# Optimization experiments

Measured on AMD Instinct MI355X. Metric: run time of the kernel, lower is better.

## Reference

```python
import jax, jax.numpy as jnp
import numpy as np

B, T, C = 8, 2048, 1024

def setup_inputs() -> dict:
    key = jax.random.key(0)
    ks = jax.random.split(key, 5)
    s_in = 1.0 / np.sqrt(C)
    s3 = 1.0 / np.sqrt(3 * C)
    return {
        'x': jax.random.normal(ks[0], (B, T, C), dtype=jnp.float32),
        'w_attn': jax.random.normal(ks[1], (C, 3 * C), dtype=jnp.float32) * s_in,
        'b_attn': jnp.zeros((3 * C,), dtype=jnp.float32),
        'w_proj': jax.random.normal(ks[2], (C, C), dtype=jnp.float32) * s_in,
        'b_proj': jnp.zeros((C,), dtype=jnp.float32),
    }

def reference(x, w_attn, b_attn, w_proj, b_proj):
    Bv, Tv, Cv = x.shape
    qkv = x @ w_attn + b_attn                      # [B,T,3C]
    q, k, v = jnp.split(qkv, 3, axis=-1)           # each [B,T,C]
    # causal additive mask, matching original -1e10 constant
    mask = jnp.where(jnp.tril(jnp.ones((Tv, Tv), dtype=jnp.bool_)), 0.0, -10000000000.0)
    attn = jnp.einsum('btc,bsc->bts', q, k) / jnp.sqrt(jnp.float32(Cv)) + mask
    attn = jax.nn.softmax(attn, axis=-1)           # [B,T,T]
    out = jnp.einsum('bts,bsc->btc', attn, v)      # [B,T,C]
    return out @ w_proj + b_proj
```

## Files before the change

### kernel.cpp

```cpp
#include <hip/hip_runtime.h>
#include <hip/hip_bf16.h>

typedef __hip_bfloat16 bf16_t;
typedef __attribute__((ext_vector_type(8))) __bf16 bf16x8;
typedef __attribute__((ext_vector_type(4))) float f32x4;
typedef __attribute__((ext_vector_type(8))) unsigned short u16x8;


__device__ __forceinline__ void gld_lds16(const void* g, void* l) {
    __builtin_amdgcn_global_load_lds(
        (const __attribute__((address_space(1))) unsigned int*)g,
        (__attribute__((address_space(3))) unsigned int*)l,
        16, 0, 0);
}

__device__ __forceinline__ unsigned short bf16_bits(float x) {
    bf16_t b = __float2bfloat16(x);
    return *reinterpret_cast<unsigned short*>(&b);
}


__global__ __launch_bounds__(256) void cvt_f32_bf16_kernel(
    const float* __restrict__ in, bf16_t* __restrict__ out, long n4) {
    long stride = (long)gridDim.x * blockDim.x;
    for (long i = (long)blockIdx.x * blockDim.x + threadIdx.x; i < n4; i += stride) {
        float4 v = reinterpret_cast<const float4*>(in)[i];
        ushort4 o;
        o.x = bf16_bits(v.x);
        o.y = bf16_bits(v.y);
        o.z = bf16_bits(v.z);
        o.w = bf16_bits(v.w);
        reinterpret_cast<ushort4*>(out)[i] = o;
    }
}


__global__ __launch_bounds__(256) void transpose_f32_bf16_kernel(
    const float* __restrict__ in, bf16_t* __restrict__ out, long ldin, long ldout) {
    __shared__ float tile[32][33];
    int c0 = blockIdx.x * 32, r0 = blockIdx.y * 32;
    int x = threadIdx.x;
#pragma unroll
    for (int yy = 0; yy < 4; ++yy) {
        int y = threadIdx.y + yy * 8;
        tile[y][x] = in[(long)(r0 + y) * ldin + c0 + x];
    }
    __syncthreads();
#pragma unroll
    for (int yy = 0; yy < 4; ++yy) {
        int y = threadIdx.y + yy * 8;
        out[(long)(c0 + y) * ldout + r0 + x] = __float2bfloat16(tile[x][y]);
    }
}

__global__ __launch_bounds__(256) void transpose_bf16_kernel(
    const bf16_t* __restrict__ in, bf16_t* __restrict__ out,
    long ldin, long ldout, long sIn, long sOut) {
    __shared__ bf16_t tile[32][33];
    in  += (long)blockIdx.z * sIn;
    out += (long)blockIdx.z * sOut;
    int c0 = blockIdx.x * 32, r0 = blockIdx.y * 32;
    int x = threadIdx.x;
#pragma unroll
    for (int yy = 0; yy < 4; ++yy) {
        int y = threadIdx.y + yy * 8;
        tile[y][x] = in[(long)(r0 + y) * ldin + c0 + x];
    }
    __syncthreads();
#pragma unroll
    for (int yy = 0; yy < 4; ++yy) {
        int y = threadIdx.y + yy * 8;
        out[(long)(c0 + y) * ldout + r0 + x] = tile[x][y];
    }
}


__global__ __launch_bounds__(512, 2) void gemm256_kernel(
    const bf16_t* __restrict__ A, const bf16_t* __restrict__ Bt,
    void* __restrict__ Cp, const float* __restrict__ bias,
    float scale, int K,
    long lda, long ldb, long ldc,
    long strideA, long strideB, long strideC,
    int mtiles, int causal_skip, int causal_klimit, int c_f32)
{
    __shared__ __align__(16) bf16_t As[2][256 * 32];
    __shared__ __align__(16) bf16_t Bs[2][256 * 32];

    int nwg = gridDim.x;
    int bid = blockIdx.x;
    int swz = (bid & 7) * (nwg >> 3) + (bid >> 3);
    int bm_t = swz % mtiles, bn_t = swz / mtiles;
    if (causal_skip && bn_t > bm_t) return;
    long bm0 = (long)bm_t * 256, bn0 = (long)bn_t * 256;

    int b = blockIdx.z;
    const char* Ab = (const char*)(A + (long)b * strideA + bm0 * lda);
    const char* Bb = (const char*)(Bt + (long)b * strideB + bn0 * ldb);
    long ldab = lda * 2, ldbb = ldb * 2;

    int tid = threadIdx.x, wave = tid >> 6, lane = tid & 63;
    int wm = wave >> 2, wn = wave & 3;
    int lr = lane & 15, kc = lane >> 4;

    int Kend = K;
    if (causal_klimit) { long kl = bm0 + 256; Kend = (kl < (long)K) ? (int)kl : K; }
    int NT = Kend >> 5;
    int NI = NT >> 1;

    int offw = wave * 1024 + lane * 16;
    int rih  = offw >> 6;
    long colswz = (long)(((lane & 3) ^ ((rih >> 1) & 3)) << 4);
    long rowbA0 = (long)rih * ldab, rowbA1 = (long)(rih + 128) * ldab;
    long rowbB0 = (long)rih * ldbb, rowbB1 = (long)(rih + 128) * ldbb;
    int ldsoff = wave * 1024;

    auto STA = [&](int t, int h, int buf) {
        gld_lds16(Ab + (h ? rowbA1 : rowbA0) + (long)t * 64 + colswz,
                  (char*)&As[buf][0] + h * 8192 + ldsoff);
    };
    auto STB = [&](int t, int h, int buf) {
        gld_lds16(Bb + (h ? rowbB1 : rowbB0) + (long)t * 64 + colswz,
                  (char*)&Bs[buf][0] + h * 8192 + ldsoff);
    };

    int aoff[8], boff[4];
#pragma unroll
    for (int m = 0; m < 8; ++m) {
        int row = wm * 128 + m * 16 + lr;
        aoff[m] = (row * 64 + kc * 16) ^ (((row >> 1) & 3) << 4);
    }
#pragma unroll
    for (int n = 0; n < 4; ++n) {
        int row = wn * 64 + n * 16 + lr;
        boff[n] = (row * 64 + kc * 16) ^ (((row >> 1) & 3) << 4);
    }

    f32x4 acc[8][4];
#pragma unroll
    for (int m = 0; m < 8; ++m)
#pragma unroll
        for (int n = 0; n < 4; ++n) acc[m][n] = (f32x4){0.f, 0.f, 0.f, 0.f};

    STA(0, 0, 0); STA(0, 1, 0);
    STB(0, 0, 0); STB(0, 1, 0);
    STB(1, 0, 1); STB(1, 1, 1);
    asm volatile("s_waitcnt vmcnt(2)" ::: "memory");
    __builtin_amdgcn_s_barrier();

    const char* As0 = (const char*)&As[0][0];
    const char* As1 = (const char*)&As[1][0];
    const char* Bs0 = (const char*)&Bs[0][0];
    const char* Bs1 = (const char*)&Bs[1][0];

    bf16x8 af[4], bfr[4];

    for (int it = 0; it < NI; ++it) {
        int o  = 2 * it + 1;
        int eN = (2 * it + 2 < NT) ? 2 * it + 2 : NT - 1;
        int oN = (2 * it + 3 < NT) ? 2 * it + 3 : NT - 1;

#pragma unroll
        for (int m = 0; m < 4; ++m) af[m] = *(const bf16x8*)(As0 + aoff[m]);
#pragma unroll
        for (int n = 0; n < 4; ++n) bfr[n] = *(const bf16x8*)(Bs0 + boff[n]);
        STA(o, 0, 1); STA(o, 1, 1);
        __builtin_amdgcn_sched_barrier(0);
        __builtin_amdgcn_s_barrier();
        asm volatile("s_waitcnt lgkmcnt(0)" ::: "memory");
        __builtin_amdgcn_sched_barrier(0);
        __builtin_amdgcn_s_setprio(1);
#pragma unroll
        for (int m = 0; m < 4; ++m)
#pragma unroll
            for (int n = 0; n < 4; ++n)
                acc[m][n] = __builtin_amdgcn_mfma_f32_16x16x32_bf16(af[m], bfr[n], acc[m][n], 0, 0, 0);
        __builtin_amdgcn_s_setprio(0);
        __builtin_amdgcn_s_barrier();

#pragma unroll
        for (int m = 0; m < 4; ++m) af[m] = *(const bf16x8*)(As0 + aoff[m + 4]);
        STB(eN, 0, 0); STB(eN, 1, 0);
        __builtin_amdgcn_sched_barrier(0);
        __builtin_amdgcn_s_barrier();
        asm volatile("s_waitcnt lgkmcnt(0)" ::: "memory");
        __builtin_amdgcn_sched_barrier(0);
        __builtin_amdgcn_s_setprio(1);
#pragma unroll
        for (int m = 0; m < 4; ++m)
#pragma unroll
            for (int n = 0; n < 4; ++n)
                acc[m + 4][n] = __builtin_amdgcn_mfma_f32_16x16x32_bf16(af[m], bfr[n], acc[m + 4][n], 0, 0, 0);
        __builtin_amdgcn_s_setprio(0);
        asm volatile("s_waitcnt vmcnt(2)" ::: "memory");
        __builtin_amdgcn_s_barrier();

#pragma unroll
        for (int m = 0; m < 4; ++m) af[m] = *(const bf16x8*)(As1 + aoff[m]);
#pragma unroll
        for (int n = 0; n < 4; ++n) bfr[n] = *(const bf16x8*)(Bs1 + boff[n]);
        STA(eN, 0, 0); STA(eN, 1, 0);
        __builtin_amdgcn_sched_barrier(0);
        __builtin_amdgcn_s_barrier();
        asm volatile("s_waitcnt lgkmcnt(0)" ::: "memory");
        __builtin_amdgcn_sched_barrier(0);
        __builtin_amdgcn_s_setprio(1);
#pragma unroll
        for (int m = 0; m < 4; ++m)
#pragma unroll
            for (int n = 0; n < 4; ++n)
                acc[m][n] = __builtin_amdgcn_mfma_f32_16x16x32_bf16(af[m], bfr[n], acc[m][n], 0, 0, 0);
        __builtin_amdgcn_s_setprio(0);
        __builtin_amdgcn_s_barrier();

#pragma unroll
        for (int m = 0; m < 4; ++m) af[m] = *(const bf16x8*)(As1 + aoff[m + 4]);
        STB(oN, 0, 1); STB(oN, 1, 1);
        __builtin_amdgcn_sched_barrier(0);
        __builtin_amdgcn_s_barrier();
        asm volatile("s_waitcnt lgkmcnt(0)" ::: "memory");
        __builtin_amdgcn_sched_barrier(0);
        __builtin_amdgcn_s_setprio(1);
#pragma unroll
        for (int m = 0; m < 4; ++m)
#pragma unroll
            for (int n = 0; n < 4; ++n)
                acc[m + 4][n] = __builtin_amdgcn_mfma_f32_16x16x32_bf16(af[m], bfr[n], acc[m + 4][n], 0, 0, 0);
        __builtin_amdgcn_s_setprio(0);
        asm volatile("s_waitcnt vmcnt(2)" ::: "memory");
        __builtin_amdgcn_s_barrier();
    }

    asm volatile("s_waitcnt vmcnt(0)" ::: "memory");

#pragma unroll
    for (int m = 0; m < 8; ++m) {
        long row = bm0 + wm * 128 + m * 16 + kc * 4;
#pragma unroll
        for (int n = 0; n < 4; ++n) {
            long col = bn0 + wn * 64 + n * 16 + lr;
            float bv = bias ? bias[col] : 0.f;
            if (c_f32) {
                float* Crow = (float*)Cp + (long)b * strideC;
#pragma unroll
                for (int r = 0; r < 4; ++r)
                    Crow[(row + r) * ldc + col] = acc[m][n][r] * scale + bv;
            } else {
                bf16_t* Crow = (bf16_t*)Cp + (long)b * strideC;
#pragma unroll
                for (int r = 0; r < 4; ++r)
                    Crow[(row + r) * ldc + col] = __float2bfloat16(acc[m][n][r] * scale + bv);
            }
        }
    }
}


__global__ __launch_bounds__(256) void softmax_causal_kernel(bf16_t* S, int T) {
    int t = blockIdx.x;
    bf16_t* row = S + ((long)blockIdx.y * T + t) * (long)T;
    int tid = threadIdx.x;
    int s0 = tid * 8;

    u16x8 raw = *reinterpret_cast<const u16x8*>(&row[s0]);
    float v[8];
#pragma unroll
    for (int j = 0; j < 8; ++j) v[j] = __uint_as_float(((unsigned)raw[j]) << 16);

    float m = -1e30f;
#pragma unroll
    for (int j = 0; j < 8; ++j)
        if (s0 + j <= t) m = fmaxf(m, v[j]);

    __shared__ float red[8];
#pragma unroll
    for (int o = 32; o; o >>= 1) m = fmaxf(m, __shfl_xor(m, o, 64));
    if ((tid & 63) == 0) red[tid >> 6] = m;
    __syncthreads();
    m = fmaxf(fmaxf(red[0], red[1]), fmaxf(red[2], red[3]));
    __syncthreads();

    float e[8];
    float sum = 0.f;
#pragma unroll
    for (int j = 0; j < 8; ++j) {
        e[j] = (s0 + j <= t) ? __expf(v[j] - m) : 0.f;
        sum += e[j];
    }
#pragma unroll
    for (int o = 32; o; o >>= 1) sum += __shfl_xor(sum, o, 64);
    if ((tid & 63) == 0) red[tid >> 6] = sum;
    __syncthreads();
    sum = red[0] + red[1] + red[2] + red[3];
    float inv = 1.f / sum;

    u16x8 outp;
#pragma unroll
    for (int j = 0; j < 8; ++j) outp[j] = bf16_bits(e[j] * inv);
    *reinterpret_cast<u16x8*>(&row[s0]) = outp;
}


extern "C" void kernel_launch(void* const* d_in, const int* in_sizes, int n_in,
                              void* d_out, int out_size, void* d_ws, size_t ws_size,
                              hipStream_t stream) {
    const int B = 8, T = 2048, C = 1024;
    const int M = B * T;
    const int N3 = 3 * C;

    const float* x      = (const float*)d_in[0];
    const float* w_attn = (const float*)d_in[1];
    const float* b_attn = (const float*)d_in[2];
    const float* w_proj = (const float*)d_in[3];
    const float* b_proj = (const float*)d_in[4];
    float* out = (float*)d_out;

    char* ws = (char*)d_ws;

    const size_t BASE_FULL = 142606336ull;
    const size_t PER_B     = 12582912ull;
    long NB = 0;
    if (ws_size >= BASE_FULL + PER_B) {
        NB = (long)((ws_size - BASE_FULL) / PER_B);
        if (NB > 8) NB = 8;
    }

    if (NB >= 1) {
        bf16_t* waT = (bf16_t*)(ws);
        bf16_t* wpT = (bf16_t*)(ws + 6291456);
        bf16_t* qkv = (bf16_t*)(ws + 8388608);
        bf16_t* xbO = (bf16_t*)(ws + 109051904);
        bf16_t* vT  = (bf16_t*)(ws + 142606336);
        bf16_t* S   = (bf16_t*)(ws + 142606336 + (size_t)NB * 4194304);

        cvt_f32_bf16_kernel<<<2048, 256, 0, stream>>>(x, xbO, (long)M * C / 4);

        transpose_f32_bf16_kernel<<<dim3(N3 / 32, C / 32, 1), dim3(32, 8), 0, stream>>>(
            w_attn, waT, N3, C);
        transpose_f32_bf16_kernel<<<dim3(C / 32, C / 32, 1), dim3(32, 8), 0, stream>>>(
            w_proj, wpT, C, C);

        gemm256_kernel<<<dim3((M / 256) * (N3 / 256), 1, 1), 512, 0, stream>>>(
            xbO, waT, qkv, b_attn, 1.0f, C,
            C, C, N3, 0, 0, 0, M / 256, 0, 0, 0);

        for (long b0 = 0; b0 < B; b0 += NB) {
            long nb = (B - b0 < NB) ? (B - b0) : NB;
            const bf16_t* qkv_c = qkv + b0 * (long)T * N3;
            bf16_t* O_c = xbO + b0 * (long)T * C;

            transpose_bf16_kernel<<<dim3(C / 32, T / 32, nb), dim3(32, 8), 0, stream>>>(
                qkv_c + 2 * C, vT, N3, T, (long)T * N3, (long)C * T);

            gemm256_kernel<<<dim3((T / 256) * (T / 256), 1, nb), 512, 0, stream>>>(
                qkv_c, qkv_c + C, S, nullptr, 0.03125f, C,
                N3, N3, T, (long)T * N3, (long)T * N3, (long)T * T, T / 256, 1, 0, 0);

            softmax_causal_kernel<<<dim3(T, nb), 256, 0, stream>>>(S, T);

            gemm256_kernel<<<dim3((T / 256) * (C / 256), 1, nb), 512, 0, stream>>>(
                S, vT, O_c, nullptr, 1.0f, T,
                T, T, C, (long)T * T, (long)C * T, (long)T * C, T / 256, 0, 1, 0);
        }

        gemm256_kernel<<<dim3((M / 256) * (C / 256), 1, 1), 512, 0, stream>>>(
            xbO, wpT, out, b_proj, 1.0f, C,
            C, C, C, 0, 0, 0, M / 256, 0, 0, 1);
    } else {
        bf16_t* waT  = (bf16_t*)(ws);
        bf16_t* wpT  = (bf16_t*)(ws + 6291456);
        bf16_t* xbO  = (bf16_t*)(ws + 8388608);
        bf16_t* qkvb = (bf16_t*)(ws + 12582912);
        bf16_t* vTb  = (bf16_t*)(ws + 25165824);
        bf16_t* Sb   = (bf16_t*)(ws + 29360128);

        transpose_f32_bf16_kernel<<<dim3(N3 / 32, C / 32, 1), dim3(32, 8), 0, stream>>>(
            w_attn, waT, N3, C);
        transpose_f32_bf16_kernel<<<dim3(C / 32, C / 32, 1), dim3(32, 8), 0, stream>>>(
            w_proj, wpT, C, C);

        for (int b = 0; b < B; ++b) {
            const float* x_b = x + (long)b * T * C;
            float* out_b = out + (long)b * T * C;

            cvt_f32_bf16_kernel<<<1024, 256, 0, stream>>>(x_b, xbO, (long)T * C / 4);

            gemm256_kernel<<<dim3((T / 256) * (N3 / 256), 1, 1), 512, 0, stream>>>(
                xbO, waT, qkvb, b_attn, 1.0f, C,
                C, C, N3, 0, 0, 0, T / 256, 0, 0, 0);

            transpose_bf16_kernel<<<dim3(C / 32, T / 32, 1), dim3(32, 8), 0, stream>>>(
                qkvb + 2 * C, vTb, N3, T, 0, 0);

            gemm256_kernel<<<dim3((T / 256) * (T / 256), 1, 1), 512, 0, stream>>>(
                qkvb, qkvb + C, Sb, nullptr, 0.03125f, C,
                N3, N3, T, 0, 0, 0, T / 256, 1, 0, 0);

            softmax_causal_kernel<<<dim3(T, 1), 256, 0, stream>>>(Sb, T);

            gemm256_kernel<<<dim3((T / 256) * (C / 256), 1, 1), 512, 0, stream>>>(
                Sb, vTb, xbO, nullptr, 1.0f, T,
                T, T, C, 0, 0, 0, T / 256, 0, 1, 0);

            gemm256_kernel<<<dim3((T / 256) * (C / 256), 1, 1), 512, 0, stream>>>(
                xbO, wpT, out_b, b_proj, 1.0f, C,
                C, C, C, 0, 0, 0, T / 256, 0, 0, 1);
        }
    }
}
```

Before: 408.1 us.

## Switch GEMM to triple-buffered LDS pipeline with two-tile prefetch distance

Replaces the double-buffered, two-tile-unrolled main loop with a three-stage ring of LDS buffers, so global-to-LDS loads for tile t+2 are issued while tile t is computed. The vmcnt wait is relaxed to allow four loads in flight, which is meant to hide more memory latency. In exchange, LDS use per block rises from 64KB to 96KB. That may cut occupancy below the two blocks per CU requested by launch_bounds, and the ring index adds some scalar work.

```diff
diff --git a/kernel.cpp b/kernel.cpp
--- a/kernel.cpp
+++ b/kernel.cpp
@@ -83,8 +83,8 @@
     long strideA, long strideB, long strideC,
     int mtiles, int causal_skip, int causal_klimit, int c_f32)
 {
-    __shared__ __align__(16) bf16_t As[2][256 * 32];
-    __shared__ __align__(16) bf16_t Bs[2][256 * 32];
+    __shared__ __align__(16) bf16_t As[3][256 * 32];
+    __shared__ __align__(16) bf16_t Bs[3][256 * 32];
 
     int nwg = gridDim.x;
     int bid = blockIdx.x;
@@ -105,7 +105,6 @@
     int Kend = K;
     if (causal_klimit) { long kl = bm0 + 256; Kend = (kl < (long)K) ? (int)kl : K; }
     int NT = Kend >> 5;
-    int NI = NT >> 1;
 
     int offw = wave * 1024 + lane * 16;
     int rih  = offw >> 6;
@@ -116,11 +115,11 @@
 
     auto STA = [&](int t, int h, int buf) {
         gld_lds16(Ab + (h ? rowbA1 : rowbA0) + (long)t * 64 + colswz,
-                  (char*)&As[buf][0] + h * 8192 + ldsoff);
+                  (char*)As + buf * 16384 + h * 8192 + ldsoff);
     };
     auto STB = [&](int t, int h, int buf) {
         gld_lds16(Bb + (h ? rowbB1 : rowbB0) + (long)t * 64 + colswz,
-                  (char*)&Bs[buf][0] + h * 8192 + ldsoff);
+                  (char*)Bs + buf * 16384 + h * 8192 + ldsoff);
     };
 
     int aoff[8], boff[4];
@@ -141,29 +140,25 @@
 #pragma unroll
         for (int n = 0; n < 4; ++n) acc[m][n] = (f32x4){0.f, 0.f, 0.f, 0.f};
 
-    STA(0, 0, 0); STA(0, 1, 0);
-    STB(0, 0, 0); STB(0, 1, 0);
-    STB(1, 0, 1); STB(1, 1, 1);
-    asm volatile("s_waitcnt vmcnt(2)" ::: "memory");
+    STA(0, 0, 0); STA(0, 1, 0); STB(0, 0, 0); STB(0, 1, 0);
+    STA(1, 0, 1); STA(1, 1, 1); STB(1, 0, 1); STB(1, 1, 1);
+    asm volatile("s_waitcnt vmcnt(4)" ::: "memory");
     __builtin_amdgcn_s_barrier();
 
-    const char* As0 = (const char*)&As[0][0];
-    const char* As1 = (const char*)&As[1][0];
-    const char* Bs0 = (const char*)&Bs[0][0];
-    const char* Bs1 = (const char*)&Bs[1][0];
-
     bf16x8 af[4], bfr[4];
-
-    for (int it = 0; it < NI; ++it) {
-        int o  = 2 * it + 1;
-        int eN = (2 * it + 2 < NT) ? 2 * it + 2 : NT - 1;
-        int oN = (2 * it + 3 < NT) ? 2 * it + 3 : NT - 1;
-
-#pragma unroll
-        for (int m = 0; m < 4; ++m) af[m] = *(const bf16x8*)(As0 + aoff[m]);
-#pragma unroll
-        for (int n = 0; n < 4; ++n) bfr[n] = *(const bf16x8*)(Bs0 + boff[n]);
-        STA(o, 0, 1); STA(o, 1, 1);
+    int cur = 0;
+
+    for (int t = 0; t < NT; ++t) {
+        int b2 = cur + 2; if (b2 >= 3) b2 -= 3;
+        int t2 = (t + 2 < NT) ? (t + 2) : t;
+        const char* Ac = (const char*)As + cur * 16384;
+        const char* Bc = (const char*)Bs + cur * 16384;
+
+#pragma unroll
+        for (int m = 0; m < 4; ++m) af[m] = *(const bf16x8*)(Ac + aoff[m]);
+#pragma unroll
+        for (int n = 0; n < 4; ++n) bfr[n] = *(const bf16x8*)(Bc + boff[n]);
+        STA(t2, 0, b2); STA(t2, 1, b2);
         __builtin_amdgcn_sched_barrier(0);
         __builtin_amdgcn_s_barrier();
         asm volatile("s_waitcnt lgkmcnt(0)" ::: "memory");
@@ -178,8 +173,8 @@
         __builtin_amdgcn_s_barrier();
 
 #pragma unroll
-        for (int m = 0; m < 4; ++m) af[m] = *(const bf16x8*)(As0 + aoff[m + 4]);
-        STB(eN, 0, 0); STB(eN, 1, 0);
+        for (int m = 0; m < 4; ++m) af[m] = *(const bf16x8*)(Ac + aoff[m + 4]);
+        STB(t2, 0, b2); STB(t2, 1, b2);
         __builtin_amdgcn_sched_barrier(0);
         __builtin_amdgcn_s_barrier();
         asm volatile("s_waitcnt lgkmcnt(0)" ::: "memory");
@@ -191,43 +186,10 @@
             for (int n = 0; n < 4; ++n)
                 acc[m + 4][n] = __builtin_amdgcn_mfma_f32_16x16x32_bf16(af[m], bfr[n], acc[m + 4][n], 0, 0, 0);
         __builtin_amdgcn_s_setprio(0);
-        asm volatile("s_waitcnt vmcnt(2)" ::: "memory");
+        asm volatile("s_waitcnt vmcnt(4)" ::: "memory");
         __builtin_amdgcn_s_barrier();
 
-#pragma unroll
-        for (int m = 0; m < 4; ++m) af[m] = *(const bf16x8*)(As1 + aoff[m]);
-#pragma unroll
-        for (int n = 0; n < 4; ++n) bfr[n] = *(const bf16x8*)(Bs1 + boff[n]);
-        STA(eN, 0, 0); STA(eN, 1, 0);
-        __builtin_amdgcn_sched_barrier(0);
-        __builtin_amdgcn_s_barrier();
-        asm volatile("s_waitcnt lgkmcnt(0)" ::: "memory");
-        __builtin_amdgcn_sched_barrier(0);
-        __builtin_amdgcn_s_setprio(1);
-#pragma unroll
-        for (int m = 0; m < 4; ++m)
-#pragma unroll
-            for (int n = 0; n < 4; ++n)
-                acc[m][n] = __builtin_amdgcn_mfma_f32_16x16x32_bf16(af[m], bfr[n], acc[m][n], 0, 0, 0);
-        __builtin_amdgcn_s_setprio(0);
-        __builtin_amdgcn_s_barrier();
-
-#pragma unroll
-        for (int m = 0; m < 4; ++m) af[m] = *(const bf16x8*)(As1 + aoff[m + 4]);
-        STB(oN, 0, 1); STB(oN, 1, 1);
-        __builtin_amdgcn_sched_barrier(0);
-        __builtin_amdgcn_s_barrier();
-        asm volatile("s_waitcnt lgkmcnt(0)" ::: "memory");
-        __builtin_amdgcn_sched_barrier(0);
-        __builtin_amdgcn_s_setprio(1);
-#pragma unroll
-        for (int m = 0; m < 4; ++m)
-#pragma unroll
-            for (int n = 0; n < 4; ++n)
-                acc[m + 4][n] = __builtin_amdgcn_mfma_f32_16x16x32_bf16(af[m], bfr[n], acc[m + 4][n], 0, 0, 0);
-        __builtin_amdgcn_s_setprio(0);
-        asm volatile("s_waitcnt vmcnt(2)" ::: "memory");
-        __builtin_amdgcn_s_barrier();
+        cur += 1; if (cur >= 3) cur -= 3;
     }
 
     asm volatile("s_waitcnt vmcnt(0)" ::: "memory");
```

Result: slower. 486.5 us (+19.2%).
